# Kernel optimization log

Measured on AMD Instinct MI355X. Metric: run time of the kernel, lower is better.

Reference implementation:

```python
import jax, jax.numpy as jnp
import numpy as np

D = 2  # NUM_DIM (spatial dimension)


def _mlp(x, params, activate_final=False):
    n = len(params)
    for i, (w, b) in enumerate(params):
        x = x @ w + b
        if i < n - 1 or activate_final:
            x = jnp.tanh(x)
    return x


def _glorot(key, shape):
    fan_in, fan_out = shape[0], shape[-1]
    lim = np.sqrt(6.0 / (fan_in + fan_out)).astype(np.float32)
    return jax.random.uniform(key, shape, jnp.float32, -lim, lim)


def setup_inputs() -> dict:
    key = jax.random.key(0)
    ks = iter(jax.random.split(key, 40))
    B, N, M, K, P, C = 4, 32, 64, 16, 128, 2
    AW, TW, W = 64, 256, 128
    inp = {}
    inp['phase_coords'] = jax.random.normal(next(ks), (B, N, 2 * D), jnp.float32)
    inp['boundary_coords'] = jax.random.normal(next(ks), (B, M, 2 * D), jnp.float32)
    inp['boundary'] = jax.random.uniform(next(ks), (B, M), jnp.float32)
    inp['boundary_weights'] = jax.random.uniform(next(ks), (B, M), jnp.float32)
    inp['position_coords'] = jax.random.normal(next(ks), (B, P, D), jnp.float32)
    inp['sigma'] = jax.random.uniform(next(ks), (B, P, C), jnp.float32)
    inp['velocity_coords'] = jax.random.normal(next(ks), (B, K, D), jnp.float32)
    inp['velocity_weights'] = jax.random.uniform(next(ks), (B, K), jnp.float32)
    inp['scattering_kernel'] = jax.random.uniform(next(ks), (B, N, K), jnp.float32)
    inp['self_scattering_kernel'] = jax.random.uniform(next(ks), (B, K, K), jnp.float32)
    # attention MLP: input 2*D + 2 (coords ++ local frame) -> [64, 64, 1]
    inp['aw0'] = _glorot(next(ks), (2 * D + 2, AW)); inp['ab0'] = jnp.zeros((AW,), jnp.float32)
    inp['aw1'] = _glorot(next(ks), (AW, AW)); inp['ab1'] = jnp.zeros((AW,), jnp.float32)
    inp['aw2'] = _glorot(next(ks), (AW, 1)); inp['ab2'] = jnp.zeros((1,), jnp.float32)
    # transport MLP: input 4*D + C -> [256, 256, 128], activate_final=True
    inp['tw0'] = _glorot(next(ks), (4 * D + C, TW)); inp['tb0'] = jnp.zeros((TW,), jnp.float32)
    inp['tw1'] = _glorot(next(ks), (TW, TW)); inp['tb1'] = jnp.zeros((TW,), jnp.float32)
    inp['tw2'] = _glorot(next(ks), (TW, W)); inp['tb2'] = jnp.zeros((W,), jnp.float32)
    # scattering modules: res_block_depth=2 -> one stacked layer + one final layer
    inp['sw0'] = _glorot(next(ks), (W, W))
    inp['sb0'] = jax.random.uniform(next(ks), (W,), jnp.float32, -0.1, 0.1)
    inp['sw1'] = _glorot(next(ks), (W, W))
    inp['sb1'] = jax.random.uniform(next(ks), (W,), jnp.float32, -0.1, 0.1)
    inp['out_w'] = jax.random.uniform(next(ks), (W,), jnp.float32, -0.1, 0.1)
    return inp


def _forward(phase_coords, boundary_coords, boundary, boundary_weights,
             position_coords, sigma, velocity_coords, velocity_weights,
             scattering_kernel, self_scattering_kernel,
             aw0, ab0, aw1, ab1, aw2, ab2,
             tw0, tb0, tw1, tb1, tw2, tb2,
             sw0, sb0, sw1, sb1, out_w):
    B, N, _ = phase_coords.shape
    M = boundary_coords.shape[1]
    K = velocity_coords.shape[1]
    P = position_coords.shape[1]
    C = sigma.shape[-1]
    K1 = K + 1  # phase velocity v plus the Nv quadrature velocities

    x, v = phase_coords[..., :D], phase_coords[..., D:]          # (B,N,D)
    xp, vp = boundary_coords[..., :D], boundary_coords[..., D:]  # (B,M,D)

    # all velocities at which the transport MLP is evaluated: (B,N,K1,D)
    vall = jnp.concatenate(
        [v[:, :, None, :],
         jnp.broadcast_to(velocity_coords[:, None, :, :], (B, N, K, D))], axis=2)

    # ---- CoefficientNet (geometry-masked MLP attention over coeff positions) ----
    coords = jnp.concatenate(
        [jnp.broadcast_to(x[:, :, None, :], (B, N, K1, D)), vall], axis=-1)  # (B,N,K1,2D)
    ang_g = vall / jnp.sqrt(jnp.sum(vall ** 2, axis=-1, keepdims=True) + 1e-16)
    rel = x[:, :, None, :] - position_coords[:, None, :, :]                 # (B,N,P,D)
    rel_dist = jnp.sqrt(jnp.sum(rel ** 2, axis=-1) + 1e-16)                 # (B,N,P)
    pos_local = jnp.einsum('bnpd,bnkd->bnkp', rel, ang_g)                   # (B,N,K1,P)
    ang_local = pos_local / (rel_dist[:, :, None, :] + 1e-8)
    frames = jnp.stack([ang_local, pos_local], axis=-1)                     # (B,N,K1,P,2)
    qk = jnp.concatenate(
        [jnp.broadcast_to(coords[:, :, :, None, :], (B, N, K1, P, 2 * D)), frames], axis=-1)
    logits = _mlp(qk, [(aw0, ab0), (aw1, ab1), (aw2, ab2)])[..., 0]         # (B,N,K1,P)
    attn_w = jax.nn.softmax(jnp.where(pos_local > 0, logits, -1e30), axis=-1)
    coeff = jnp.exp(-jnp.einsum('bnkp,bpc->bnkc', attn_w, sigma))           # (B,N,K1,C)

    # ---- TransportModule: MLP + exp over (B,N,M,K1) ----
    t_in = jnp.concatenate([
        jnp.broadcast_to(x[:, :, None, None, :], (B, N, M, K1, D)),
        jnp.broadcast_to(vall[:, :, None, :, :], (B, N, M, K1, D)),
        jnp.broadcast_to(xp[:, None, :, None, :], (B, N, M, K1, D)),
        jnp.broadcast_to(vp[:, None, :, None, :], (B, N, M, K1, D)),
        jnp.broadcast_to(coeff[:, :, None, :, :], (B, N, M, K1, C)),
    ], axis=-1)
    g = jnp.exp(_mlp(t_in, [(tw0, tb0), (tw1, tb1), (tw2, tb2)], activate_final=True))
    act_v = g[:, :, :, 0, :]       # (B,N,M,W)  at the phase velocity
    act_vstar = g[:, :, :, 1:, :]  # (B,N,M,K,W) at the quadrature velocities

    rw_v = (1.0 - scattering_kernel) * velocity_weights[:, None, :]        # (B,N,K)
    rw_vs = (1.0 - self_scattering_kernel) * velocity_weights[:, None, :]  # (B,K,K)

    def scat_v(act, sw, sb):
        res = jnp.einsum('bnk,bnmkw->bnmw', rw_v, act)
        return jnp.tanh(jnp.einsum('iw,bnmw->bnmi', sw, res) + sb)

    def scat_vs(act, sw, sb):
        res = jnp.einsum('bij,bnmjw->bnmiw', rw_vs, act)
        return jnp.tanh(jnp.einsum('iw,bnmkw->bnmki', sw, res) + sb)

    # layer_stack block (res_block_depth - 1 = 1 layer, shared params within the layer)
    new_v = act_v + scat_v(act_vstar, sw0, sb0)
    act_vstar = act_vstar + scat_vs(act_vstar, sw0, sb0)
    act_v = new_v
    # final scattering module (fresh params) updating act_v with res_weights_v
    green = act_v + scat_v(act_vstar, sw1, sb1)

    gdot = jnp.einsum('bnmw,w->bnm', green, out_w)
    # quadrature over boundary points
    return jnp.einsum('bnm,bm->bn', gdot, boundary * boundary_weights)


def reference(phase_coords, boundary_coords, boundary, boundary_weights,
              position_coords, sigma, velocity_coords, velocity_weights,
              scattering_kernel, self_scattering_kernel,
              aw0, ab0, aw1, ab1, aw2, ab2,
              tw0, tb0, tw1, tb1, tw2, tb2,
              sw0, sb0, sw1, sb1, out_w):
    return _forward(phase_coords, boundary_coords, boundary, boundary_weights,
                    position_coords, sigma, velocity_coords, velocity_weights,
                    scattering_kernel, self_scattering_kernel,
                    aw0, ab0, aw1, ab1, aw2, ab2,
                    tw0, tb0, tw1, tb1, tw2, tb2,
                    sw0, sb0, sw1, sb1, out_w)
```

## Files before the change

kernel.cpp:

```cpp
#include <hip/hip_runtime.h>
#include <hip/hip_bf16.h>

#define BB 4
#define NN 32
#define MM 64
#define KK 16
#define KK1 17
#define PP 128
#define CC 2

typedef unsigned short ushort_t;
typedef unsigned int uint32;
typedef __attribute__((ext_vector_type(8))) short bhalf8;
typedef __attribute__((ext_vector_type(4))) float floatx4;

__device__ __forceinline__ float fast_tanh(float x) {
    float e = __expf(2.0f * x);
    return 1.0f - 2.0f / (e + 1.0f);
}
__device__ __forceinline__ ushort_t f2b(float f) {
    uint32 u = __float_as_uint(f);
    return (ushort_t)((u + 0x8000u) >> 16);
}
__device__ __forceinline__ float b2f(ushort_t h) {
    return __uint_as_float(((uint32)h) << 16);
}

__global__ void prep_kernel(const float* __restrict__ tw0, const float* __restrict__ tw1,
                            const float* __restrict__ tw2, const float* __restrict__ sw0,
                            const float* __restrict__ sw1, const float* __restrict__ aw0,
                            const float* __restrict__ aw1, const float* __restrict__ tb0,
                            const float* __restrict__ bcoord,
                            ushort_t* __restrict__ W1t, ushort_t* __restrict__ W2t,
                            ushort_t* __restrict__ S0t, ushort_t* __restrict__ S1t,
                            ushort_t* __restrict__ W0a, ushort_t* __restrict__ W1a,
                            ushort_t* __restrict__ w_ws) {
    int i = blockIdx.x * 256 + threadIdx.x;
    if (i < 65536) {
        int nn = i >> 8, k = i & 255;
        W1t[i] = f2b(tw1[k * 256 + nn]);
    } else if (i < 98304) {
        int j = i - 65536; int nn = j >> 8, k = j & 255;
        W2t[j] = f2b(tw2[k * 128 + nn]);
    } else if (i < 114688) {
        S0t[i - 98304] = f2b(sw0[i - 98304]);
    } else if (i < 131072) {
        S1t[i - 114688] = f2b(sw1[i - 114688]);
    } else if (i < 133120) {
        int j = i - 131072; int nn = j >> 5, k = j & 31;
        W0a[j] = (k < 6) ? f2b(aw0[k * 64 + nn]) : (ushort_t)0;
    } else if (i < 137216) {
        int j = i - 133120; int nn = j >> 6, k = j & 63;
        W1a[j] = f2b(aw1[k * 64 + nn]);
    } else if (i < 202752) {
        int j = i - 137216;
        int m = j >> 8, c = j & 255;
        float v = bcoord[m * 4 + 0] * tw0[4 * 256 + c]
                + bcoord[m * 4 + 1] * tw0[5 * 256 + c]
                + bcoord[m * 4 + 2] * tw0[6 * 256 + c]
                + bcoord[m * 4 + 3] * tw0[7 * 256 + c]
                + tb0[c];
        w_ws[j] = f2b(v);
    }
}

#define AH0S 72

__global__ __launch_bounds__(128, 4) void attn_kernel(
    const float* __restrict__ phase, const float* __restrict__ posc,
    const float* __restrict__ sigma, const float* __restrict__ velc,
    const ushort_t* __restrict__ W0a, const ushort_t* __restrict__ W1a,
    const float* __restrict__ ab0, const float* __restrict__ ab1,
    const float* __restrict__ aw2, const float* __restrict__ ab2,
    const float* __restrict__ tw0, ushort_t* __restrict__ u_ws)
{
    __shared__ __align__(16) ushort_t sAH[128 * AH0S];
    __shared__ float sPL[128];
    __shared__ float sLG[128];
    __shared__ float s_red[8];

    const int tid = threadIdx.x;
    const int wave = tid >> 6;
    const int lane = tid & 63;
    const int lrow = lane & 15;
    const int lkg  = lane >> 4;

    const int blk = blockIdx.x;
    const int b = blk / (NN * KK1);
    const int rem = blk % (NN * KK1);
    const int n = rem / KK1;
    const int k = rem % KK1;

    float x0, x1, va0, va1;
    {
        const int p = tid;
        x0 = phase[(b * NN + n) * 4 + 0];
        x1 = phase[(b * NN + n) * 4 + 1];
        if (k == 0) { va0 = phase[(b * NN + n) * 4 + 2]; va1 = phase[(b * NN + n) * 4 + 3]; }
        else { va0 = velc[(b * KK + (k - 1)) * 2 + 0]; va1 = velc[(b * KK + (k - 1)) * 2 + 1]; }
        const float inv = rsqrtf(va0 * va0 + va1 * va1 + 1e-16f);
        const float ag0 = va0 * inv, ag1 = va1 * inv;
        const float px = posc[(b * PP + p) * 2 + 0];
        const float py = posc[(b * PP + p) * 2 + 1];
        const float r0 = x0 - px, r1 = x1 - py;
        const float rd = sqrtf(r0 * r0 + r1 * r1 + 1e-16f);
        const float pl = r0 * ag0 + r1 * ag1;
        const float al = pl / (rd + 1e-8f);
        sPL[p] = pl;
        bhalf8 f0;
        f0[0] = (short)f2b(x0); f0[1] = (short)f2b(x1);
        f0[2] = (short)f2b(va0); f0[3] = (short)f2b(va1);
        f0[4] = (short)f2b(al); f0[5] = (short)f2b(pl);
        f0[6] = 0; f0[7] = 0;
        bhalf8 z = {0, 0, 0, 0, 0, 0, 0, 0};
        *(bhalf8*)&sAH[p * 32 + 0] = f0;
        *(bhalf8*)&sAH[p * 32 + 8] = z;
        *(bhalf8*)&sAH[p * 32 + 16] = z;
        *(bhalf8*)&sAH[p * 32 + 24] = z;
    }
    __syncthreads();

    {
        float b0v[4];
        #pragma unroll
        for (int j = 0; j < 4; ++j) b0v[j] = ab0[j * 16 + lrow];
        bhalf8 a[4];
        #pragma unroll
        for (int mtl = 0; mtl < 4; ++mtl)
            a[mtl] = *(const bhalf8*)&sAH[(wave * 64 + mtl * 16 + lrow) * 32 + lkg * 8];
        __syncthreads();
        #pragma unroll
        for (int j = 0; j < 4; ++j) {
            bhalf8 bf = *(const bhalf8*)(W0a + (j * 16 + lrow) * 32 + lkg * 8);
            #pragma unroll
            for (int mtl = 0; mtl < 4; ++mtl) {
                floatx4 c = {0.f, 0.f, 0.f, 0.f};
                c = __builtin_amdgcn_mfma_f32_16x16x32_bf16(a[mtl], bf, c, 0, 0, 0);
                #pragma unroll
                for (int q = 0; q < 4; ++q) {
                    int row = wave * 64 + mtl * 16 + lkg * 4 + q;
                    sAH[row * AH0S + j * 16 + lrow] = f2b(fast_tanh(c[q] + b0v[j]));
                }
            }
        }
    }
    __syncthreads();

    {
        float b1v[4], w2v[4];
        #pragma unroll
        for (int j = 0; j < 4; ++j) { b1v[j] = ab1[j * 16 + lrow]; w2v[j] = aw2[j * 16 + lrow]; }
        bhalf8 a0[4], a1[4];
        #pragma unroll
        for (int mtl = 0; mtl < 4; ++mtl) {
            int base = (wave * 64 + mtl * 16 + lrow) * AH0S;
            a0[mtl] = *(const bhalf8*)&sAH[base + lkg * 8];
            a1[mtl] = *(const bhalf8*)&sAH[base + 32 + lkg * 8];
        }
        float s[4][4];
        #pragma unroll
        for (int mtl = 0; mtl < 4; ++mtl)
            #pragma unroll
            for (int q = 0; q < 4; ++q) s[mtl][q] = 0.0f;
        #pragma unroll
        for (int j = 0; j < 4; ++j) {
            bhalf8 bf0 = *(const bhalf8*)(W1a + (j * 16 + lrow) * 64 + lkg * 8);
            bhalf8 bf1 = *(const bhalf8*)(W1a + (j * 16 + lrow) * 64 + 32 + lkg * 8);
            #pragma unroll
            for (int mtl = 0; mtl < 4; ++mtl) {
                floatx4 c = {0.f, 0.f, 0.f, 0.f};
                c = __builtin_amdgcn_mfma_f32_16x16x32_bf16(a0[mtl], bf0, c, 0, 0, 0);
                c = __builtin_amdgcn_mfma_f32_16x16x32_bf16(a1[mtl], bf1, c, 0, 0, 0);
                #pragma unroll
                for (int q = 0; q < 4; ++q)
                    s[mtl][q] += fast_tanh(c[q] + b1v[j]) * w2v[j];
            }
        }
        #pragma unroll
        for (int mask = 1; mask <= 8; mask <<= 1)
            #pragma unroll
            for (int mtl = 0; mtl < 4; ++mtl)
                #pragma unroll
                for (int q = 0; q < 4; ++q)
                    s[mtl][q] += __shfl_xor(s[mtl][q], mask, 64);
        if (lrow == 0) {
            #pragma unroll
            for (int mtl = 0; mtl < 4; ++mtl)
                #pragma unroll
                for (int q = 0; q < 4; ++q)
                    sLG[wave * 64 + mtl * 16 + lkg * 4 + q] = s[mtl][q];
        }
    }
    __syncthreads();

    {
        const int p = tid;
        const float ml = (sPL[p] > 0.0f) ? (sLG[p] + ab2[0]) : -1e30f;
        const int wid = wave;
        float mv = ml;
        for (int o = 32; o > 0; o >>= 1) mv = fmaxf(mv, __shfl_xor(mv, o, 64));
        if (lane == 0) s_red[wid] = mv;
        __syncthreads();
        mv = fmaxf(s_red[0], s_red[1]);

        const float ew = __expf(ml - mv);
        float sv = ew;
        for (int o = 32; o > 0; o >>= 1) sv += __shfl_xor(sv, o, 64);
        if (lane == 0) s_red[2 + wid] = sv;
        __syncthreads();
        sv = s_red[2] + s_red[3];
        const float attn = ew / sv;

        float s0 = attn * sigma[(b * PP + p) * 2 + 0];
        float s1 = attn * sigma[(b * PP + p) * 2 + 1];
        for (int o = 32; o > 0; o >>= 1) { s0 += __shfl_xor(s0, o, 64); s1 += __shfl_xor(s1, o, 64); }
        if (lane == 0) { s_red[4 + wid] = s0; s_red[6 + wid] = s1; }
        __syncthreads();

        const float cc0 = __expf(-(s_red[4] + s_red[5]));
        const float cc1 = __expf(-(s_red[6] + s_red[7]));
        const int ubase = ((b * NN + n) * KK1 + k) * 256;
        for (int cc = tid; cc < 256; cc += 128) {
            float uv = x0 * tw0[cc] + x1 * tw0[256 + cc]
                     + va0 * tw0[512 + cc] + va1 * tw0[768 + cc]
                     + cc0 * tw0[2048 + cc] + cc1 * tw0[2304 + cc];
            u_ws[ubase + cc] = f2b(uv);
        }
    }
}

#define H0S  136
#define H1S  264
#define GTSs 40
#define AS2S 136
#define V2S  40

#define U_H0A  0
#define U_GTS  0
#define U_GV   5128
#define U_NEWV 5384
#define U_A2S  5640
#define U_H1A  6152
#define U_AS2  6152
#define U_A3   6152
#define U_AS   15128
#define U_V2T  15128
#define F_BBW  10128
#define F_RED  10130

__global__ __launch_bounds__(256, 4) void transport_kernel(
    const float* __restrict__ boundary, const float* __restrict__ bweights,
    const float* __restrict__ vweights, const float* __restrict__ scat,
    const float* __restrict__ selfscat,
    const ushort_t* __restrict__ W1t, const ushort_t* __restrict__ W2t,
    const ushort_t* __restrict__ S0t, const ushort_t* __restrict__ S1t,
    const float* __restrict__ tb1, const float* __restrict__ tb2,
    const float* __restrict__ sb0, const float* __restrict__ sb1,
    const float* __restrict__ outw,
    const ushort_t* __restrict__ u_ws, const ushort_t* __restrict__ w_ws,
    float* __restrict__ out)
{
    __shared__ __align__(16) ushort_t smem[20268];
    float* smf = (float*)smem;

    const int tid = threadIdx.x;
    const int wave = tid >> 6;
    const int lane = tid & 63;
    const int lrow = lane & 15;
    const int lkg  = lane >> 4;

    const int blk = blockIdx.x;
    const int b  = blk >> 10;
    const int n  = (blk >> 5) & 31;
    const int mg = blk & 31;
    const int m0 = mg * 2;
    const int bn = b * NN + n;

    if (tid < 2)
        smf[F_BBW + tid] = boundary[b * MM + m0 + tid] * bweights[b * MM + m0 + tid];

    for (int idx = tid; idx < 17 * 32; idx += 256) {
        int i = idx >> 5, c = idx & 31;
        float val = 0.0f;
        if (c < 16) {
            float vw = vweights[b * KK + c];
            val = (i < 16) ? (1.0f - selfscat[(b * KK + i) * KK + c]) * vw
                           : (1.0f - scat[bn * KK + c]) * vw;
        }
        smem[U_AS + idx] = f2b(val);
    }

    floatx4 c1[4][3];
    #pragma unroll
    for (int j = 0; j < 4; ++j)
        #pragma unroll
        for (int mt = 0; mt < 3; ++mt) c1[j][mt] = (floatx4){0.f, 0.f, 0.f, 0.f};

    for (int chunk = 0; chunk < 2; ++chunk) {
        if (chunk) __syncthreads();
        for (int idx = tid; idx < 34 * 16; idx += 256) {
            int row = idx >> 4, oct = idx & 15;
            int ml = (row >= 17);
            int k = row - ml * 17;
            bhalf8 uu = *(const bhalf8*)(u_ws + (bn * KK1 + k) * 256 + chunk * 128 + oct * 8);
            bhalf8 ww = *(const bhalf8*)(w_ws + (b * MM + m0 + ml) * 256 + chunk * 128 + oct * 8);
            bhalf8 hh;
            #pragma unroll
            for (int jj = 0; jj < 8; ++jj)
                hh[jj] = (short)f2b(fast_tanh(b2f((ushort_t)uu[jj]) + b2f((ushort_t)ww[jj])));
            *(bhalf8*)&smem[U_H0A + row * H0S + oct * 8] = hh;
        }
        __syncthreads();
        #pragma unroll
        for (int ksl = 0; ksl < 4; ++ksl) {
            bhalf8 a[3];
            #pragma unroll
            for (int mt = 0; mt < 3; ++mt)
                a[mt] = *(const bhalf8*)&smem[U_H0A + (mt * 16 + lrow) * H0S + ksl * 32 + lkg * 8];
            #pragma unroll
            for (int j = 0; j < 4; ++j) {
                bhalf8 bf = *(const bhalf8*)(W1t + ((4 * wave + j) * 16 + lrow) * 256
                                             + chunk * 128 + ksl * 32 + lkg * 8);
                #pragma unroll
                for (int mt = 0; mt < 3; ++mt)
                    c1[j][mt] = __builtin_amdgcn_mfma_f32_16x16x32_bf16(a[mt], bf, c1[j][mt], 0, 0, 0);
            }
        }
    }
    {
        #pragma unroll
        for (int j = 0; j < 4; ++j) {
            float bb = tb1[(4 * wave + j) * 16 + lrow];
            #pragma unroll
            for (int mt = 0; mt < 3; ++mt)
                #pragma unroll
                for (int q = 0; q < 4; ++q) {
                    int row = mt * 16 + lkg * 4 + q;
                    if (row < 34)
                        smem[U_H1A + row * H1S + (4 * wave + j) * 16 + lrow] =
                            f2b(fast_tanh(c1[j][mt][q] + bb));
                }
        }
    }
    __syncthreads();

    for (int idx = tid; idx < 1032; idx += 256) {
        int pos = (idx < 1024) ? ((idx >> 3) * GTSs + 32 + (idx & 7)) : (5120 + idx - 1024);
        smem[U_GTS + pos] = 0;
    }
    {
        floatx4 c2[2][3];
        #pragma unroll
        for (int j = 0; j < 2; ++j)
            #pragma unroll
            for (int mt = 0; mt < 3; ++mt) c2[j][mt] = (floatx4){0.f, 0.f, 0.f, 0.f};
        #pragma unroll
        for (int ks = 0; ks < 8; ++ks) {
            bhalf8 a[3];
            #pragma unroll
            for (int mt = 0; mt < 3; ++mt)
                a[mt] = *(const bhalf8*)&smem[U_H1A + (mt * 16 + lrow) * H1S + ks * 32 + lkg * 8];
            #pragma unroll
            for (int j = 0; j < 2; ++j) {
                bhalf8 bf = *(const bhalf8*)(W2t + ((2 * wave + j) * 16 + lrow) * 256 + ks * 32 + lkg * 8);
                #pragma unroll
                for (int mt = 0; mt < 3; ++mt)
                    c2[j][mt] = __builtin_amdgcn_mfma_f32_16x16x32_bf16(a[mt], bf, c2[j][mt], 0, 0, 0);
            }
        }
        #pragma unroll
        for (int j = 0; j < 2; ++j) {
            float bb = tb2[(2 * wave + j) * 16 + lrow];
            #pragma unroll
            for (int mt = 0; mt < 3; ++mt)
                #pragma unroll
                for (int q = 0; q < 4; ++q) {
                    int row = mt * 16 + lkg * 4 + q;
                    if (row < 34) {
                        int ml = (row >= 17);
                        int k = row - ml * 17;
                        int col = (2 * wave + j) * 16 + lrow;
                        float g = __expf(fast_tanh(c2[j][mt][q] + bb));
                        if (k == 0) smem[U_GV + ml * 128 + col] = f2b(g);
                        else        smem[U_GTS + col * GTSs + ml * 16 + (k - 1)] = f2b(g);
                    }
                }
        }
    }
    __syncthreads();

    for (int idx = tid; idx < 512; idx += 256) {
        int r = idx >> 5, c = idx & 31;
        smem[U_A2S + idx] = ((c >> 4) == r) ? smem[U_AS + 16 * 32 + (c & 15)] : (ushort_t)0;
    }
    {
        bhalf8 a0 = *(const bhalf8*)&smem[U_AS + lrow * 32 + lkg * 8];
        bhalf8 a1 = *(const bhalf8*)&smem[U_AS + (16 + lrow) * 32 + lkg * 8];
        for (int m = 0; m < 2; ++m) {
            #pragma unroll
            for (int j = 0; j < 2; ++j) {
                int nt = 2 * wave + j;
                bhalf8 bf = *(const bhalf8*)&smem[U_GTS + (nt * 16 + lrow) * GTSs + m * 16 + lkg * 8];
                #pragma unroll
                for (int mt = 0; mt < 2; ++mt) {
                    floatx4 c = {0.f, 0.f, 0.f, 0.f};
                    c = __builtin_amdgcn_mfma_f32_16x16x32_bf16(mt ? a1 : a0, bf, c, 0, 0, 0);
                    #pragma unroll
                    for (int q = 0; q < 4; ++q) {
                        int ic = mt * 16 + lkg * 4 + q;
                        if (ic < 17) {
                            int r2 = (ic == 16) ? m * 17 : m * 17 + 1 + ic;
                            smem[U_AS2 + r2 * AS2S + nt * 16 + lrow] = f2b(c[q]);
                        }
                    }
                }
            }
        }
    }
    __syncthreads();

    {
        floatx4 c3[2][3];
        #pragma unroll
        for (int j = 0; j < 2; ++j)
            #pragma unroll
            for (int mt = 0; mt < 3; ++mt) c3[j][mt] = (floatx4){0.f, 0.f, 0.f, 0.f};
        #pragma unroll
        for (int ks = 0; ks < 4; ++ks) {
            bhalf8 a[3];
            #pragma unroll
            for (int mt = 0; mt < 3; ++mt)
                a[mt] = *(const bhalf8*)&smem[U_AS2 + (mt * 16 + lrow) * AS2S + ks * 32 + lkg * 8];
            #pragma unroll
            for (int j = 0; j < 2; ++j) {
                bhalf8 bf = *(const bhalf8*)(S0t + ((2 * wave + j) * 16 + lrow) * 128 + ks * 32 + lkg * 8);
                #pragma unroll
                for (int mt = 0; mt < 3; ++mt)
                    c3[j][mt] = __builtin_amdgcn_mfma_f32_16x16x32_bf16(a[mt], bf, c3[j][mt], 0, 0, 0);
            }
        }
        #pragma unroll
        for (int j = 0; j < 2; ++j) {
            float bb = sb0[(2 * wave + j) * 16 + lrow];
            #pragma unroll
            for (int mt = 0; mt < 3; ++mt)
                #pragma unroll
                for (int q = 0; q < 4; ++q) {
                    int r2 = mt * 16 + lkg * 4 + q;
                    if (r2 < 34) {
                        int m = (r2 >= 17);
                        int i2 = r2 - m * 17;
                        int col = (2 * wave + j) * 16 + lrow;
                        float val = fast_tanh(c3[j][mt][q] + bb);
                        if (i2 == 0) {
                            smem[U_NEWV + m * 128 + col] =
                                f2b(b2f(smem[U_GV + m * 128 + col]) + val);
                        } else {
                            int j2 = i2 - 1;
                            smem[U_V2T + col * V2S + m * 16 + j2] =
                                f2b(b2f(smem[U_GTS + col * GTSs + m * 16 + j2]) + val);
                        }
                    }
                }
        }
    }
    __syncthreads();

    {
        bhalf8 a = *(const bhalf8*)&smem[U_A2S + lrow * 32 + lkg * 8];
        #pragma unroll
        for (int j = 0; j < 2; ++j) {
            int nt = 2 * wave + j;
            bhalf8 bf = *(const bhalf8*)&smem[U_V2T + (nt * 16 + lrow) * V2S + lkg * 8];
            floatx4 c = {0.f, 0.f, 0.f, 0.f};
            c = __builtin_amdgcn_mfma_f32_16x16x32_bf16(a, bf, c, 0, 0, 0);
            #pragma unroll
            for (int q = 0; q < 4; ++q) {
                int r = lkg * 4 + q;
                smem[U_A3 + r * AS2S + nt * 16 + lrow] = f2b(c[q]);
            }
        }
    }
    __syncthreads();

    float acc = 0.0f;
    {
        bhalf8 a[4];
        #pragma unroll
        for (int ks = 0; ks < 4; ++ks)
            a[ks] = *(const bhalf8*)&smem[U_A3 + lrow * AS2S + ks * 32 + lkg * 8];
        #pragma unroll
        for (int j = 0; j < 2; ++j) {
            int nt = 2 * wave + j;
            float s1v = sb1[nt * 16 + lrow];
            float owv = outw[nt * 16 + lrow];
            floatx4 c = {0.f, 0.f, 0.f, 0.f};
            #pragma unroll
            for (int ks = 0; ks < 4; ++ks) {
                bhalf8 bf = *(const bhalf8*)(S1t + (nt * 16 + lrow) * 128 + ks * 32 + lkg * 8);
                c = __builtin_amdgcn_mfma_f32_16x16x32_bf16(a[ks], bf, c, 0, 0, 0);
            }
            #pragma unroll
            for (int q = 0; q < 4; ++q) {
                int r = lkg * 4 + q;
                if (r < 2) {
                    int col = nt * 16 + lrow;
                    float green = b2f(smem[U_NEWV + r * 128 + col]) + fast_tanh(c[q] + s1v);
                    acc += green * owv * smf[F_BBW + r];
                }
            }
        }
    }
    for (int o = 32; o > 0; o >>= 1) acc += __shfl_xor(acc, o, 64);
    if (lane == 0) smf[F_RED + wave] = acc;
    __syncthreads();
    if (tid == 0) {
        float tot = smf[F_RED + 0] + smf[F_RED + 1] + smf[F_RED + 2] + smf[F_RED + 3];
        atomicAdd(&out[bn], tot);
    }
}

extern "C" void kernel_launch(void* const* d_in, const int* in_sizes, int n_in,
                              void* d_out, int out_size, void* d_ws, size_t ws_size,
                              hipStream_t stream) {
    const float* phase    = (const float*)d_in[0];
    const float* bcoord   = (const float*)d_in[1];
    const float* boundary = (const float*)d_in[2];
    const float* bweights = (const float*)d_in[3];
    const float* posc     = (const float*)d_in[4];
    const float* sigma    = (const float*)d_in[5];
    const float* velc     = (const float*)d_in[6];
    const float* vweights = (const float*)d_in[7];
    const float* scat     = (const float*)d_in[8];
    const float* selfscat = (const float*)d_in[9];
    const float* aw0 = (const float*)d_in[10];
    const float* ab0 = (const float*)d_in[11];
    const float* aw1 = (const float*)d_in[12];
    const float* ab1 = (const float*)d_in[13];
    const float* aw2 = (const float*)d_in[14];
    const float* ab2 = (const float*)d_in[15];
    const float* tw0 = (const float*)d_in[16];
    const float* tb0 = (const float*)d_in[17];
    const float* tw1 = (const float*)d_in[18];
    const float* tb1 = (const float*)d_in[19];
    const float* tw2 = (const float*)d_in[20];
    const float* tb2 = (const float*)d_in[21];
    const float* sw0 = (const float*)d_in[22];
    const float* sb0 = (const float*)d_in[23];
    const float* sw1 = (const float*)d_in[24];
    const float* sb1 = (const float*)d_in[25];
    const float* outw = (const float*)d_in[26];

    float* out = (float*)d_out;
    char* ws = (char*)d_ws;
    ushort_t* W1t  = (ushort_t*)(ws + 0);
    ushort_t* W2t  = (ushort_t*)(ws + 131072);
    ushort_t* S0t  = (ushort_t*)(ws + 196608);
    ushort_t* S1t  = (ushort_t*)(ws + 229376);
    ushort_t* W0a  = (ushort_t*)(ws + 262144);
    ushort_t* W1a  = (ushort_t*)(ws + 266240);
    ushort_t* u_ws = (ushort_t*)(ws + 274432);
    ushort_t* w_ws = (ushort_t*)(ws + 1388544);

    hipMemsetAsync(d_out, 0, (size_t)out_size * sizeof(float), stream);

    prep_kernel<<<792, 256, 0, stream>>>(tw0, tw1, tw2, sw0, sw1, aw0, aw1, tb0, bcoord,
                                         W1t, W2t, S0t, S1t, W0a, W1a, w_ws);

    attn_kernel<<<BB * NN * KK1, 128, 0, stream>>>(
        phase, posc, sigma, velc, W0a, W1a, ab0, ab1, aw2, ab2, tw0, u_ws);

    transport_kernel<<<BB * NN * 32, 256, 0, stream>>>(
        boundary, bweights, vweights, scat, selfscat,
        W1t, W2t, S0t, S1t, tb1, tb2, sb0, sb1, outw, u_ws, w_ws, out);
}
```

Before: 285.8 us.

## Restructure transport MLP into chunked layer-1/layer-2 pipeline with fp32 workspaces

Stores u_ws/w_ws intermediates in fp32 instead of bf16 and computes the full layer-0 tanh activations into shared memory once. It then chunks layer 1 by output columns and feeds each chunk straight into a partial layer-2 accumulation, so only half of the hidden layer is held in LDS at a time. The LDS footprint shrinks, allowing launch bounds of 5 blocks per CU instead of 4. In exchange it doubles global traffic for the intermediates, adds a sync per chunk, and keeps extra accumulators live in registers.

Measured after the change: 312.8 us. 1.09x slower.

```diff
diff --git a/kernel.cpp b/kernel.cpp
--- a/kernel.cpp
+++ b/kernel.cpp
@@ -34,7 +34,7 @@
                             ushort_t* __restrict__ W1t, ushort_t* __restrict__ W2t,
                             ushort_t* __restrict__ S0t, ushort_t* __restrict__ S1t,
                             ushort_t* __restrict__ W0a, ushort_t* __restrict__ W1a,
-                            ushort_t* __restrict__ w_ws) {
+                            float* __restrict__ w_ws) {
     int i = blockIdx.x * 256 + threadIdx.x;
     if (i < 65536) {
         int nn = i >> 8, k = i & 255;
@@ -60,7 +60,7 @@
                 + bcoord[m * 4 + 2] * tw0[6 * 256 + c]
                 + bcoord[m * 4 + 3] * tw0[7 * 256 + c]
                 + tb0[c];
-        w_ws[j] = f2b(v);
+        w_ws[j] = v;
     }
 }
 
@@ -72,7 +72,7 @@
     const ushort_t* __restrict__ W0a, const ushort_t* __restrict__ W1a,
     const float* __restrict__ ab0, const float* __restrict__ ab1,
     const float* __restrict__ aw2, const float* __restrict__ ab2,
-    const float* __restrict__ tw0, ushort_t* __restrict__ u_ws)
+    const float* __restrict__ tw0, float* __restrict__ u_ws)
 {
     __shared__ __align__(16) ushort_t sAH[128 * AH0S];
     __shared__ float sPL[128];
@@ -224,31 +224,31 @@
             float uv = x0 * tw0[cc] + x1 * tw0[256 + cc]
                      + va0 * tw0[512 + cc] + va1 * tw0[768 + cc]
                      + cc0 * tw0[2048 + cc] + cc1 * tw0[2304 + cc];
-            u_ws[ubase + cc] = f2b(uv);
-        }
-    }
-}
-
-#define H0S  136
-#define H1S  264
+            u_ws[ubase + cc] = uv;
+        }
+    }
+}
+
+#define H0S  264
+#define H1S  136
 #define GTSs 40
 #define AS2S 136
 #define V2S  40
 
 #define U_H0A  0
+#define U_H1A  8976
+#define U_AS   13600
 #define U_GTS  0
-#define U_GV   5128
-#define U_NEWV 5384
-#define U_A2S  5640
-#define U_H1A  6152
-#define U_AS2  6152
-#define U_A3   6152
-#define U_AS   15128
-#define U_V2T  15128
-#define F_BBW  10128
-#define F_RED  10130
-
-__global__ __launch_bounds__(256, 4) void transport_kernel(
+#define U_GV   5120
+#define U_NEWV 5376
+#define U_AS2  5632
+#define U_V2T  10256
+#define U_A2S  15376
+#define U_A3   0
+#define F_BBW  7944
+#define F_RED  7946
+
+__global__ __launch_bounds__(256, 5) void transport_kernel(
     const float* __restrict__ boundary, const float* __restrict__ bweights,
     const float* __restrict__ vweights, const float* __restrict__ scat,
     const float* __restrict__ selfscat,
@@ -257,10 +257,10 @@
     const float* __restrict__ tb1, const float* __restrict__ tb2,
     const float* __restrict__ sb0, const float* __restrict__ sb1,
     const float* __restrict__ outw,
-    const ushort_t* __restrict__ u_ws, const ushort_t* __restrict__ w_ws,
+    const float* __restrict__ u_ws, const float* __restrict__ w_ws,
     float* __restrict__ out)
 {
-    __shared__ __align__(16) ushort_t smem[20268];
+    __shared__ __align__(16) ushort_t smem[15900];
     float* smf = (float*)smem;
 
     const int tid = threadIdx.x;
@@ -290,87 +290,93 @@
         smem[U_AS + idx] = f2b(val);
     }
 
-    floatx4 c1[4][3];
+    for (int idx = tid; idx < 34 * 32; idx += 256) {
+        int row = idx >> 5, oct = idx & 31;
+        int ml = (row >= 17);
+        int k = row - ml * 17;
+        const float4* up = (const float4*)(u_ws + (bn * KK1 + k) * 256 + oct * 8);
+        const float4* wp = (const float4*)(w_ws + (b * MM + m0 + ml) * 256 + oct * 8);
+        float4 u0 = up[0], u1 = up[1];
+        float4 w0 = wp[0], w1 = wp[1];
+        bhalf8 hh;
+        hh[0] = (short)f2b(fast_tanh(u0.x + w0.x));
+        hh[1] = (short)f2b(fast_tanh(u0.y + w0.y));
+        hh[2] = (short)f2b(fast_tanh(u0.z + w0.z));
+        hh[3] = (short)f2b(fast_tanh(u0.w + w0.w));
+        hh[4] = (short)f2b(fast_tanh(u1.x + w1.x));
+        hh[5] = (short)f2b(fast_tanh(u1.y + w1.y));
+        hh[6] = (short)f2b(fast_tanh(u1.z + w1.z));
+        hh[7] = (short)f2b(fast_tanh(u1.w + w1.w));
+        *(bhalf8*)&smem[U_H0A + row * H0S + oct * 8] = hh;
+    }
+    __syncthreads();
+
+    floatx4 c2[2][3];
     #pragma unroll
-    for (int j = 0; j < 4; ++j)
-        #pragma unroll
-        for (int mt = 0; mt < 3; ++mt) c1[j][mt] = (floatx4){0.f, 0.f, 0.f, 0.f};
+    for (int j = 0; j < 2; ++j)
+        #pragma unroll
+        for (int mt = 0; mt < 3; ++mt) c2[j][mt] = (floatx4){0.f, 0.f, 0.f, 0.f};
 
     for (int chunk = 0; chunk < 2; ++chunk) {
         if (chunk) __syncthreads();
-        for (int idx = tid; idx < 34 * 16; idx += 256) {
-            int row = idx >> 4, oct = idx & 15;
-            int ml = (row >= 17);
-            int k = row - ml * 17;
-            bhalf8 uu = *(const bhalf8*)(u_ws + (bn * KK1 + k) * 256 + chunk * 128 + oct * 8);
-            bhalf8 ww = *(const bhalf8*)(w_ws + (b * MM + m0 + ml) * 256 + chunk * 128 + oct * 8);
-            bhalf8 hh;
-            #pragma unroll
-            for (int jj = 0; jj < 8; ++jj)
-                hh[jj] = (short)f2b(fast_tanh(b2f((ushort_t)uu[jj]) + b2f((ushort_t)ww[jj])));
-            *(bhalf8*)&smem[U_H0A + row * H0S + oct * 8] = hh;
-        }
-        __syncthreads();
-        #pragma unroll
-        for (int ksl = 0; ksl < 4; ++ksl) {
+        floatx4 c1[2][3];
+        #pragma unroll
+        for (int j = 0; j < 2; ++j)
+            #pragma unroll
+            for (int mt = 0; mt < 3; ++mt) c1[j][mt] = (floatx4){0.f, 0.f, 0.f, 0.f};
+        #pragma unroll
+        for (int ks = 0; ks < 8; ++ks) {
             bhalf8 a[3];
             #pragma unroll
             for (int mt = 0; mt < 3; ++mt)
-                a[mt] = *(const bhalf8*)&smem[U_H0A + (mt * 16 + lrow) * H0S + ksl * 32 + lkg * 8];
-            #pragma unroll
-            for (int j = 0; j < 4; ++j) {
-                bhalf8 bf = *(const bhalf8*)(W1t + ((4 * wave + j) * 16 + lrow) * 256
-                                             + chunk * 128 + ksl * 32 + lkg * 8);
+                a[mt] = *(const bhalf8*)&smem[U_H0A + (mt * 16 + lrow) * H0S + ks * 32 + lkg * 8];
+            #pragma unroll
+            for (int j = 0; j < 2; ++j) {
+                int colt = chunk * 8 + wave * 2 + j;
+                bhalf8 bf = *(const bhalf8*)(W1t + (colt * 16 + lrow) * 256 + ks * 32 + lkg * 8);
                 #pragma unroll
                 for (int mt = 0; mt < 3; ++mt)
                     c1[j][mt] = __builtin_amdgcn_mfma_f32_16x16x32_bf16(a[mt], bf, c1[j][mt], 0, 0, 0);
             }
         }
-    }
-    {
-        #pragma unroll
-        for (int j = 0; j < 4; ++j) {
-            float bb = tb1[(4 * wave + j) * 16 + lrow];
+        #pragma unroll
+        for (int j = 0; j < 2; ++j) {
+            const int lcol = (wave * 2 + j) * 16 + lrow;
+            const float bb = tb1[chunk * 128 + lcol];
             #pragma unroll
             for (int mt = 0; mt < 3; ++mt)
                 #pragma unroll
                 for (int q = 0; q < 4; ++q) {
                     int row = mt * 16 + lkg * 4 + q;
                     if (row < 34)
-                        smem[U_H1A + row * H1S + (4 * wave + j) * 16 + lrow] =
-                            f2b(fast_tanh(c1[j][mt][q] + bb));
+                        smem[U_H1A + row * H1S + lcol] = f2b(fast_tanh(c1[j][mt][q] + bb));
                 }
         }
-    }
-    __syncthreads();
-
-    for (int idx = tid; idx < 1032; idx += 256) {
-        int pos = (idx < 1024) ? ((idx >> 3) * GTSs + 32 + (idx & 7)) : (5120 + idx - 1024);
-        smem[U_GTS + pos] = 0;
-    }
-    {
-        floatx4 c2[2][3];
-        #pragma unroll
-        for (int j = 0; j < 2; ++j)
-            #pragma unroll
-            for (int mt = 0; mt < 3; ++mt) c2[j][mt] = (floatx4){0.f, 0.f, 0.f, 0.f};
-        #pragma unroll
-        for (int ks = 0; ks < 8; ++ks) {
+        __syncthreads();
+        #pragma unroll
+        for (int ks2 = 0; ks2 < 4; ++ks2) {
             bhalf8 a[3];
             #pragma unroll
             for (int mt = 0; mt < 3; ++mt)
-                a[mt] = *(const bhalf8*)&smem[U_H1A + (mt * 16 + lrow) * H1S + ks * 32 + lkg * 8];
+                a[mt] = *(const bhalf8*)&smem[U_H1A + (mt * 16 + lrow) * H1S + ks2 * 32 + lkg * 8];
             #pragma unroll
             for (int j = 0; j < 2; ++j) {
-                bhalf8 bf = *(const bhalf8*)(W2t + ((2 * wave + j) * 16 + lrow) * 256 + ks * 32 + lkg * 8);
+                bhalf8 bf = *(const bhalf8*)(W2t + ((wave * 2 + j) * 16 + lrow) * 256
+                                             + chunk * 128 + ks2 * 32 + lkg * 8);
                 #pragma unroll
                 for (int mt = 0; mt < 3; ++mt)
                     c2[j][mt] = __builtin_amdgcn_mfma_f32_16x16x32_bf16(a[mt], bf, c2[j][mt], 0, 0, 0);
             }
         }
+    }
+
+    for (int idx = tid; idx < 1024; idx += 256)
+        smem[U_GTS + (idx >> 3) * GTSs + 32 + (idx & 7)] = 0;
+    {
         #pragma unroll
         for (int j = 0; j < 2; ++j) {
-            float bb = tb2[(2 * wave + j) * 16 + lrow];
+            const int col = (wave * 2 + j) * 16 + lrow;
+            const float bb = tb2[col];
             #pragma unroll
             for (int mt = 0; mt < 3; ++mt)
                 #pragma unroll
@@ -379,7 +385,6 @@
                     if (row < 34) {
                         int ml = (row >= 17);
                         int k = row - ml * 17;
-                        int col = (2 * wave + j) * 16 + lrow;
                         float g = __expf(fast_tanh(c2[j][mt][q] + bb));
                         if (k == 0) smem[U_GV + ml * 128 + col] = f2b(g);
                         else        smem[U_GTS + col * GTSs + ml * 16 + (k - 1)] = f2b(g);
@@ -441,7 +446,8 @@
         }
         #pragma unroll
         for (int j = 0; j < 2; ++j) {
-            float bb = sb0[(2 * wave + j) * 16 + lrow];
+            const int col = (2 * wave + j) * 16 + lrow;
+            const float bb = sb0[col];
             #pragma unroll
             for (int mt = 0; mt < 3; ++mt)
                 #pragma unroll
@@ -450,7 +456,6 @@
                     if (r2 < 34) {
                         int m = (r2 >= 17);
                         int i2 = r2 - m * 17;
-                        int col = (2 * wave + j) * 16 + lrow;
                         float val = fast_tanh(c3[j][mt][q] + bb);
                         if (i2 == 0) {
                             smem[U_NEWV + m * 128 + col] =
@@ -559,8 +564,8 @@
     ushort_t* S1t  = (ushort_t*)(ws + 229376);
     ushort_t* W0a  = (ushort_t*)(ws + 262144);
     ushort_t* W1a  = (ushort_t*)(ws + 266240);
-    ushort_t* u_ws = (ushort_t*)(ws + 274432);
-    ushort_t* w_ws = (ushort_t*)(ws + 1388544);
+    float* u_ws    = (float*)(ws + 274432);
+    float* w_ws    = (float*)(ws + 2502656);
 
     hipMemsetAsync(d_out, 0, (size_t)out_size * sizeof(float), stream);
 
```
